# Kernel tuning notes

Measured on AMD Instinct MI355X. Metric: run time of the kernel, lower is better.

## Reference

```python
import jax, jax.numpy as jnp
import numpy as np

B, N, M = 8, 8192, 8192


def setup_inputs() -> dict:
    key = jax.random.key(0)
    k1, k2 = jax.random.split(key)
    xyz1 = jax.random.normal(k1, (B, N, 3), dtype=jnp.float32)
    xyz2 = jax.random.normal(k2, (B, M, 3), dtype=jnp.float32)
    return {"xyz1": xyz1, "xyz2": xyz2}


def _chamfer_one(a, b):
    # a: [N,3], b: [M,3]
    aa = jnp.sum(a * a, axis=-1)          # [N]
    bb = jnp.sum(b * b, axis=-1)          # [M]
    # squared pairwise distances: [N, M]
    D = aa[:, None] + bb[None, :] - 2.0 * (a @ b.T)
    i1 = jnp.argmin(D, axis=1)            # [N] nearest in b for each a
    i2 = jnp.argmin(D, axis=0)            # [M] nearest in a for each b
    # recompute exact squared distance via gather (numerically exact, matches
    # the CUDA kernel which accumulates (a-b)^2 directly)
    d1 = jnp.sum((a - b[i1]) ** 2, axis=-1)  # [N]
    d2 = jnp.sum((b - a[i2]) ** 2, axis=-1)  # [M]
    return d1, d2


def reference(xyz1, xyz2):
    # lax.map over batch keeps only one [N,M] distance matrix live at a time
    dist1, dist2 = jax.lax.map(lambda ab: _chamfer_one(ab[0], ab[1]), (xyz1, xyz2))
    return dist1, dist2  # ([B,N], [B,M]) squared min distances, both directions
```

## Files before the change

kernel.cpp:

```cpp
#include <hip/hip_runtime.h>
#include <hip/hip_bf16.h>
#include <float.h>

#define B_      8
#define N_      8192
#define M_      8192
#define NSIDE   (B_ * N_)
#define NTOT    (2 * NSIDE)
#define THREADS 256
#define PM      2
#define BSPLIT  4
#define BCHUNK  (M_ / BSPLIT)
#define NTILE   (BCHUNK / 32)
#define NBLOCKS (2 * BSPLIT * (N_ / THREADS) * B_)

#define BIAS    128.0f

typedef _Float16 f16;
typedef f16   f16x8  __attribute__((ext_vector_type(8)));
typedef float f32x16 __attribute__((ext_vector_type(16)));

__global__ void prep_kernel(const float* __restrict__ xyz1,
                            const float* __restrict__ xyz2,
                            f16* __restrict__ Bpack,
                            float* __restrict__ aw,
                            float* __restrict__ out,
                            int n1, int n_total) {
    int i = blockIdx.x * blockDim.x + threadIdx.x;
    if (i >= n_total) return;
    const float* s = (i < n1) ? (xyz1 + 3 * i) : (xyz2 + 3 * (i - n1));
    float x = s[0], y = s[1], z = s[2];
    float w = fmaf(x, x, fmaf(y, y, z * z));
    f16 xh = (f16)x, yh = (f16)y, zh = (f16)z;
    f16 xl = (f16)(x - (float)xh);
    f16 yl = (f16)(y - (float)yh);
    f16 zl = (f16)(z - (float)zh);
    f16 wh = (f16)w;
    f16 wl = (f16)(w - (float)wh);
    f16x8 b0 = {wh, wl, xh, xl, xh, yh, yl, yh};
    f16x8 b1 = {zh, zl, zh, (f16)BIAS, (f16)0, (f16)0, (f16)0, (f16)0};
    *(f16x8*)(Bpack + (size_t)i * 16 + 0) = b0;
    *(f16x8*)(Bpack + (size_t)i * 16 + 8) = b1;
    aw[i]  = w;
    out[i] = FLT_MAX;
}

__global__ void init_kernel(float* __restrict__ out, int n) {
    int i = blockIdx.x * blockDim.x + threadIdx.x;
    if (i < n) out[i] = FLT_MAX;
}

static __device__ __forceinline__ unsigned umin2(unsigned a, unsigned b) {
    return a < b ? a : b;
}

__global__ __launch_bounds__(THREADS, 2) void chamfer_mfma32(
    const float* __restrict__ xyz1,
    const float* __restrict__ xyz2,
    const f16*  __restrict__ Bpack,
    const float* __restrict__ aw,
    float* __restrict__ out)
{
    int bid = blockIdx.x;
    int dir   = bid & 1;   bid >>= 1;
    int bs    = bid & (BSPLIT - 1); bid >>= 2;
    int ab    = bid & 31;  bid >>= 5;
    int batch = bid;

    const int lane = threadIdx.x & 63;
    const int wv   = threadIdx.x >> 6;
    const int g    = lane >> 5;
    const int c    = lane & 31;

    const int aoff = dir ? NSIDE : 0;
    const int boff = dir ? 0 : NSIDE;
    const int abase = batch * N_ + ab * THREADS + wv * (PM * 32);

    const float* axyz = (dir ? xyz2 : xyz1);

    f16x8 af[PM];
#pragma unroll
    for (int t = 0; t < PM; ++t) {
        int pa = abase + t * 32 + c;
        const float* s = axyz + 3 * (size_t)pa;
        float x = s[0], y = s[1], z = s[2];
        f16 xh = (f16)x, yh = (f16)y, zh = (f16)z;
        f16 xl = (f16)(x - (float)xh);
        f16 yl = (f16)(y - (float)yh);
        f16 zl = (f16)(z - (float)zh);
        f16 x2 = (f16)(-2.0f * (float)xh), x2l = (f16)(-2.0f * (float)xl);
        f16 y2 = (f16)(-2.0f * (float)yh), y2l = (f16)(-2.0f * (float)yl);
        f16 z2 = (f16)(-2.0f * (float)zh), z2l = (f16)(-2.0f * (float)zl);
        f16x8 lo = {(f16)1.0f, (f16)1.0f, x2, x2, x2l, y2, y2, y2l};
        f16x8 hi = {z2, z2, z2l, (f16)1.0f, (f16)0, (f16)0, (f16)0, (f16)0};
        af[t] = (g == 0) ? lo : hi;
    }

    const f16* Bp = Bpack + (size_t)(boff + batch * M_ + bs * BCHUNK) * 16;
    const f16* blane = Bp + (size_t)c * 16 + g * 8;

    unsigned m[PM][16];
#pragma unroll
    for (int t = 0; t < PM; ++t)
#pragma unroll
        for (int i = 0; i < 16; ++i) m[t][i] = 0x7F7FFFFFu;

    const f32x16 zero16 = {0.f,0.f,0.f,0.f,0.f,0.f,0.f,0.f,
                           0.f,0.f,0.f,0.f,0.f,0.f,0.f,0.f};

    f16x8 b0 = *(const f16x8*)(blane + 0 * 512);
    f16x8 b1 = *(const f16x8*)(blane + 1 * 512);
    f16x8 b2 = *(const f16x8*)(blane + 2 * 512);
    f16x8 b3 = *(const f16x8*)(blane + 3 * 512);
    for (int it = 0; it < NTILE; it += 2) {
        f16x8 c0 = b0, c1 = b1;
        b0 = b2; b1 = b3;
        b2 = *(const f16x8*)(blane + (size_t)(it + 4) * 512);
        b3 = *(const f16x8*)(blane + (size_t)(it + 5) * 512);
#pragma unroll
        for (int t = 0; t < PM; ++t) {
            f32x16 d0 = __builtin_amdgcn_mfma_f32_32x32x16_f16(af[t], c0, zero16, 0, 0, 0);
            f32x16 d1 = __builtin_amdgcn_mfma_f32_32x32x16_f16(af[t], c1, zero16, 0, 0, 0);
#pragma unroll
            for (int i = 0; i < 16; ++i) {
                unsigned u0 = __float_as_uint(d0[i]);
                unsigned u1 = __float_as_uint(d1[i]);
                m[t][i] = umin2(m[t][i], umin2(u0, u1));
            }
        }
    }

    const float* awp = aw + aoff;
    float* o = out + aoff;
#pragma unroll
    for (int t = 0; t < PM; ++t) {
        unsigned mm[16];
#pragma unroll
        for (int i = 0; i < 16; ++i) mm[i] = m[t][i];
#pragma unroll
        for (int s = 1; s < 32; s <<= 1) {
#pragma unroll
            for (int i = 0; i < 16; ++i)
                mm[i] = umin2(mm[i], (unsigned)__shfl_xor((int)mm[i], s));
        }
        unsigned uval = mm[0];
#pragma unroll
        for (int r = 1; r < 16; ++r) uval = (c == r) ? mm[r] : uval;
        if (c < 16) {
            int row = abase + t * 32 + (c & 3) + 8 * (c >> 2) + 4 * g;
            float val = __uint_as_float(uval) - BIAS;
            float dd = fmaxf(awp[row] + val, 0.0f);
            atomicMin((unsigned int*)(o + row), __float_as_uint(dd));
        }
    }
}

#define FP      8
#define FSPLIT  8
#define FCHUNK  (M_ / FSPLIT)
#define FAPB    (THREADS * FP)
#define FATILES (N_ / FAPB)
#define FNBLOCKS (2 * FSPLIT * FATILES * B_)
__global__ __launch_bounds__(THREADS) void chamfer_raw(
    const float* __restrict__ xyz1,
    const float* __restrict__ xyz2,
    float* __restrict__ out)
{
    int bid = blockIdx.x;
    int dir   = bid & 1;                 bid >>= 1;
    int chunk = bid & (FSPLIT - 1);      bid /= FSPLIT;
    int atile = bid & (FATILES - 1);     bid /= FATILES;
    int batch = bid;

    const float* A  = dir ? xyz2 : xyz1;
    const float* Bp = dir ? xyz1 : xyz2;
    float* o = out + (dir ? (B_ * N_) : 0);

    const int a0 = batch * N_ + atile * FAPB + threadIdx.x;

    float ax2[FP], ay2[FP], az2[FP], aww[FP], mm[FP];
#pragma unroll
    for (int p = 0; p < FP; ++p) {
        int idx = a0 + p * THREADS;
        float x = A[3 * idx + 0];
        float y = A[3 * idx + 1];
        float z = A[3 * idx + 2];
        ax2[p] = -2.0f * x;
        ay2[p] = -2.0f * y;
        az2[p] = -2.0f * z;
        aww[p] = fmaf(x, x, fmaf(y, y, z * z));
        mm[p]  = FLT_MAX;
    }

    const float* bp = Bp + 3 * (batch * M_ + chunk * FCHUNK);
#pragma unroll 2
    for (int j = 0; j < FCHUNK; j += 2) {
        float b0x = bp[3 * j + 0], b0y = bp[3 * j + 1], b0z = bp[3 * j + 2];
        float b1x = bp[3 * j + 3], b1y = bp[3 * j + 4], b1z = bp[3 * j + 5];
        float b0w = fmaf(b0x, b0x, fmaf(b0y, b0y, b0z * b0z));
        float b1w = fmaf(b1x, b1x, fmaf(b1y, b1y, b1z * b1z));
#pragma unroll
        for (int p = 0; p < FP; ++p) {
            float t0 = fmaf(ax2[p], b0x, b0w);
            t0 = fmaf(ay2[p], b0y, t0);
            t0 = fmaf(az2[p], b0z, t0);
            float t1 = fmaf(ax2[p], b1x, b1w);
            t1 = fmaf(ay2[p], b1y, t1);
            t1 = fmaf(az2[p], b1z, t1);
            mm[p] = fminf(mm[p], fminf(t0, t1));
        }
    }

#pragma unroll
    for (int p = 0; p < FP; ++p) {
        float d = fmaxf(aww[p] + mm[p], 0.0f);
        atomicMin((unsigned int*)(o + a0 + p * THREADS), __float_as_uint(d));
    }
}

extern "C" void kernel_launch(void* const* d_in, const int* in_sizes, int n_in,
                              void* d_out, int out_size, void* d_ws, size_t ws_size,
                              hipStream_t stream) {
    const float* xyz1 = (const float*)d_in[0];
    const float* xyz2 = (const float*)d_in[1];
    float* out = (float*)d_out;

    const size_t bpack_bytes = (size_t)NTOT * 32;
    const size_t need = bpack_bytes + (size_t)NTOT * 4 + 16384;
    if (ws_size >= need) {
        f16*   Bpack = (f16*)d_ws;
        float* aw    = (float*)((char*)d_ws + bpack_bytes);
        prep_kernel<<<(NTOT + 255) / 256, 256, 0, stream>>>(
            xyz1, xyz2, Bpack, aw, out, NSIDE, NTOT);
        chamfer_mfma32<<<NBLOCKS, THREADS, 0, stream>>>(xyz1, xyz2, Bpack, aw, out);
    } else {
        init_kernel<<<(NTOT + 255) / 256, 256, 0, stream>>>(out, NTOT);
        chamfer_raw<<<FNBLOCKS, THREADS, 0, stream>>>(xyz1, xyz2, out);
    }
}
```

Baseline: 49.29 us.

## Compute both chamfer directions from one distance tile with shared-memory column mins

Instead of launching separate block sets for each direction, each block computes the full squared-distance tile once, folding the A-point norm into the MFMA via extra K slots, and reduces it both along rows (per A point) and along columns (per B point). Column minima are combined across waves through LDS atomics and then pushed to global with atomicMin. This halves the MFMA work and the B-packing, at the cost of extra per-tile in-register reductions, cross-lane shuffles, and LDS atomics inside the hot loop. Occupancy hint is raised to 4 blocks per CU.

Result: slower. 57.85 us (+17.4%).

```diff
diff --git a/kernel.cpp b/kernel.cpp
--- a/kernel.cpp
+++ b/kernel.cpp
@@ -12,7 +12,7 @@
 #define BSPLIT  4
 #define BCHUNK  (M_ / BSPLIT)
 #define NTILE   (BCHUNK / 32)
-#define NBLOCKS (2 * BSPLIT * (N_ / THREADS) * B_)
+#define NBLOCKS (BSPLIT * (N_ / THREADS) * B_)
 
 #define BIAS    128.0f
 
@@ -20,28 +20,27 @@
 typedef f16   f16x8  __attribute__((ext_vector_type(8)));
 typedef float f32x16 __attribute__((ext_vector_type(16)));
 
-__global__ void prep_kernel(const float* __restrict__ xyz1,
-                            const float* __restrict__ xyz2,
+__global__ void prep_kernel(const float* __restrict__ xyz2,
                             f16* __restrict__ Bpack,
-                            float* __restrict__ aw,
                             float* __restrict__ out,
-                            int n1, int n_total) {
+                            int n_pack, int n_total) {
     int i = blockIdx.x * blockDim.x + threadIdx.x;
     if (i >= n_total) return;
-    const float* s = (i < n1) ? (xyz1 + 3 * i) : (xyz2 + 3 * (i - n1));
-    float x = s[0], y = s[1], z = s[2];
-    float w = fmaf(x, x, fmaf(y, y, z * z));
-    f16 xh = (f16)x, yh = (f16)y, zh = (f16)z;
-    f16 xl = (f16)(x - (float)xh);
-    f16 yl = (f16)(y - (float)yh);
-    f16 zl = (f16)(z - (float)zh);
-    f16 wh = (f16)w;
-    f16 wl = (f16)(w - (float)wh);
-    f16x8 b0 = {wh, wl, xh, xl, xh, yh, yl, yh};
-    f16x8 b1 = {zh, zl, zh, (f16)BIAS, (f16)0, (f16)0, (f16)0, (f16)0};
-    *(f16x8*)(Bpack + (size_t)i * 16 + 0) = b0;
-    *(f16x8*)(Bpack + (size_t)i * 16 + 8) = b1;
-    aw[i]  = w;
+    if (i < n_pack) {
+        const float* s = xyz2 + 3 * (size_t)i;
+        float x = s[0], y = s[1], z = s[2];
+        float w = fmaf(x, x, fmaf(y, y, z * z));
+        f16 xh = (f16)x, yh = (f16)y, zh = (f16)z;
+        f16 xl = (f16)(x - (float)xh);
+        f16 yl = (f16)(y - (float)yh);
+        f16 zl = (f16)(z - (float)zh);
+        f16 wh = (f16)w;
+        f16 wl = (f16)(w - (float)wh);
+        f16x8 b0 = {wh, wl, xh, xl, xh, yh, yl, yh};
+        f16x8 b1 = {zh, zl, zh, (f16)BIAS, (f16)1.0f, (f16)1.0f, (f16)0, (f16)0};
+        *(f16x8*)(Bpack + (size_t)i * 16 + 0) = b0;
+        *(f16x8*)(Bpack + (size_t)i * 16 + 8) = b1;
+    }
     out[i] = FLT_MAX;
 }
 
@@ -54,15 +53,14 @@
     return a < b ? a : b;
 }
 
-__global__ __launch_bounds__(THREADS, 2) void chamfer_mfma32(
+__global__ __launch_bounds__(THREADS, 4) void chamfer_sym(
     const float* __restrict__ xyz1,
-    const float* __restrict__ xyz2,
     const f16*  __restrict__ Bpack,
-    const float* __restrict__ aw,
     float* __restrict__ out)
 {
+    __shared__ unsigned scol[BCHUNK];
+
     int bid = blockIdx.x;
-    int dir   = bid & 1;   bid >>= 1;
     int bs    = bid & (BSPLIT - 1); bid >>= 2;
     int ab    = bid & 31;  bid >>= 5;
     int batch = bid;
@@ -72,31 +70,32 @@
     const int g    = lane >> 5;
     const int c    = lane & 31;
 
-    const int aoff = dir ? NSIDE : 0;
-    const int boff = dir ? 0 : NSIDE;
+    for (int i = threadIdx.x; i < BCHUNK; i += THREADS)
+        scol[i] = 0x7F7FFFFFu;
+
     const int abase = batch * N_ + ab * THREADS + wv * (PM * 32);
-
-    const float* axyz = (dir ? xyz2 : xyz1);
 
     f16x8 af[PM];
 #pragma unroll
     for (int t = 0; t < PM; ++t) {
         int pa = abase + t * 32 + c;
-        const float* s = axyz + 3 * (size_t)pa;
+        const float* s = xyz1 + 3 * (size_t)pa;
         float x = s[0], y = s[1], z = s[2];
+        float w = fmaf(x, x, fmaf(y, y, z * z));
         f16 xh = (f16)x, yh = (f16)y, zh = (f16)z;
         f16 xl = (f16)(x - (float)xh);
         f16 yl = (f16)(y - (float)yh);
         f16 zl = (f16)(z - (float)zh);
+        f16 awh = (f16)w, awl = (f16)(w - (float)awh);
         f16 x2 = (f16)(-2.0f * (float)xh), x2l = (f16)(-2.0f * (float)xl);
         f16 y2 = (f16)(-2.0f * (float)yh), y2l = (f16)(-2.0f * (float)yl);
         f16 z2 = (f16)(-2.0f * (float)zh), z2l = (f16)(-2.0f * (float)zl);
         f16x8 lo = {(f16)1.0f, (f16)1.0f, x2, x2, x2l, y2, y2, y2l};
-        f16x8 hi = {z2, z2, z2l, (f16)1.0f, (f16)0, (f16)0, (f16)0, (f16)0};
+        f16x8 hi = {z2, z2, z2l, (f16)1.0f, awh, awl, (f16)0, (f16)0};
         af[t] = (g == 0) ? lo : hi;
     }
 
-    const f16* Bp = Bpack + (size_t)(boff + batch * M_ + bs * BCHUNK) * 16;
+    const f16* Bp = Bpack + (size_t)(batch * M_ + bs * BCHUNK) * 16;
     const f16* blane = Bp + (size_t)c * 16 + g * 8;
 
     unsigned m[PM][16];
@@ -107,6 +106,8 @@
 
     const f32x16 zero16 = {0.f,0.f,0.f,0.f,0.f,0.f,0.f,0.f,
                            0.f,0.f,0.f,0.f,0.f,0.f,0.f,0.f};
+
+    __syncthreads();
 
     f16x8 b0 = *(const f16x8*)(blane + 0 * 512);
     f16x8 b1 = *(const f16x8*)(blane + 1 * 512);
@@ -118,20 +119,30 @@
         b2 = *(const f16x8*)(blane + (size_t)(it + 4) * 512);
         b3 = *(const f16x8*)(blane + (size_t)(it + 5) * 512);
 #pragma unroll
-        for (int t = 0; t < PM; ++t) {
-            f32x16 d0 = __builtin_amdgcn_mfma_f32_32x32x16_f16(af[t], c0, zero16, 0, 0, 0);
-            f32x16 d1 = __builtin_amdgcn_mfma_f32_32x32x16_f16(af[t], c1, zero16, 0, 0, 0);
+        for (int q = 0; q < 2; ++q) {
+            f16x8 ct = q ? c1 : c0;
+            f32x16 dA = __builtin_amdgcn_mfma_f32_32x32x16_f16(af[0], ct, zero16, 0, 0, 0);
+            f32x16 dB = __builtin_amdgcn_mfma_f32_32x32x16_f16(af[1], ct, zero16, 0, 0, 0);
+            unsigned w0[16];
 #pragma unroll
             for (int i = 0; i < 16; ++i) {
-                unsigned u0 = __float_as_uint(d0[i]);
-                unsigned u1 = __float_as_uint(d1[i]);
-                m[t][i] = umin2(m[t][i], umin2(u0, u1));
+                unsigned uA = __float_as_uint(dA[i]);
+                unsigned uB = __float_as_uint(dB[i]);
+                m[0][i] = umin2(m[0][i], uA);
+                m[1][i] = umin2(m[1][i], uB);
+                w0[i] = umin2(uA, uB);
             }
-        }
-    }
-
-    const float* awp = aw + aoff;
-    float* o = out + aoff;
+#pragma unroll
+            for (int s = 8; s >= 1; s >>= 1)
+#pragma unroll
+                for (int i = 0; i < s; ++i)
+                    w0[i] = umin2(w0[i], w0[i + s]);
+            unsigned v = umin2(w0[0], (unsigned)__shfl_xor((int)w0[0], 32));
+            if (lane < 32)
+                atomicMin(&scol[(it + q) * 32 + c], v);
+        }
+    }
+
 #pragma unroll
     for (int t = 0; t < PM; ++t) {
         unsigned mm[16];
@@ -149,9 +160,16 @@
         if (c < 16) {
             int row = abase + t * 32 + (c & 3) + 8 * (c >> 2) + 4 * g;
             float val = __uint_as_float(uval) - BIAS;
-            float dd = fmaxf(awp[row] + val, 0.0f);
-            atomicMin((unsigned int*)(o + row), __float_as_uint(dd));
-        }
+            float dd = fmaxf(val, 0.0f);
+            atomicMin((unsigned int*)(out + row), __float_as_uint(dd));
+        }
+    }
+
+    __syncthreads();
+    float* o2 = out + NSIDE + batch * M_ + bs * BCHUNK;
+    for (int ci = threadIdx.x; ci < BCHUNK; ci += THREADS) {
+        float val = __uint_as_float(scol[ci]) - BIAS;
+        atomicMin((unsigned int*)(o2 + ci), __float_as_uint(fmaxf(val, 0.0f)));
     }
 }
 
@@ -225,14 +243,13 @@
     const float* xyz2 = (const float*)d_in[1];
     float* out = (float*)d_out;
 
-    const size_t bpack_bytes = (size_t)NTOT * 32;
-    const size_t need = bpack_bytes + (size_t)NTOT * 4 + 16384;
+    const size_t bpack_bytes = (size_t)NSIDE * 32;
+    const size_t need = bpack_bytes + 16384;
     if (ws_size >= need) {
-        f16*   Bpack = (f16*)d_ws;
-        float* aw    = (float*)((char*)d_ws + bpack_bytes);
+        f16* Bpack = (f16*)d_ws;
         prep_kernel<<<(NTOT + 255) / 256, 256, 0, stream>>>(
-            xyz1, xyz2, Bpack, aw, out, NSIDE, NTOT);
-        chamfer_mfma32<<<NBLOCKS, THREADS, 0, stream>>>(xyz1, xyz2, Bpack, aw, out);
+            xyz2, Bpack, out, NSIDE, NTOT);
+        chamfer_sym<<<NBLOCKS, THREADS, 0, stream>>>(xyz1, Bpack, out);
     } else {
         init_kernel<<<(NTOT + 255) / 256, 256, 0, stream>>>(out, NTOT);
         chamfer_raw<<<FNBLOCKS, THREADS, 0, stream>>>(xyz1, xyz2, out);
```
